# Optimization experiments

Hardware: AMD Instinct MI355X
Metric: run time of the kernel (lower is better)

## Reference

```python
import jax, jax.numpy as jnp
import numpy as np

B, V, F = 32, 1024, 16
A, P, NF = 32, 64, 128
C = P + A  # propagated feature width after concat with edge weights
D_OUT_IN = F + A + 2 * A * C  # 6192, input dim of output Dense


def setup_inputs() -> dict:
    key = jax.random.key(0)
    ks = jax.random.split(key, 4)
    return {
        "x": jax.random.normal(ks[0], (B, V, F), dtype=jnp.float32),
        "W_flr": jax.random.normal(ks[1], (F, P), dtype=jnp.float32) * (1.0 / np.sqrt(F)),
        "b_flr": jnp.zeros((P,), dtype=jnp.float32),
        "W_s": jax.random.normal(ks[2], (F, A), dtype=jnp.float32) * (1.0 / np.sqrt(F)),
        "b_s": jnp.zeros((A,), dtype=jnp.float32),
        "W_out": jax.random.normal(ks[3], (D_OUT_IN, NF), dtype=jnp.float32) * (1.0 / np.sqrt(D_OUT_IN)),
        "b_out": jnp.zeros((NF,), dtype=jnp.float32),
    }


def reference(x, W_flr, b_flr, W_s, b_s, W_out, b_out):
    # Per-vertex transforms
    feat = x @ W_flr + b_flr                      # (B,V,P)
    dist = x @ W_s + b_s                          # (B,V,A)
    ew = jnp.exp(-jnp.square(dist))               # (B,V,A) edge weights vertex->aggregator
    f = jnp.concatenate([feat, ew], axis=-1)      # (B,V,C)

    # Weighted broadcast then vertex-axis reduction (aggregator gather)
    w = jnp.transpose(ew, (0, 2, 1))              # (B,A,V)
    prod = w[..., None] * f[:, None, :, :]        # (B,A,V,C)
    agg_max = jnp.max(prod, axis=2)               # (B,A,C)
    agg_mean = jnp.mean(prod, axis=2)             # (B,A,C)
    agg = jnp.concatenate([agg_max, agg_mean], axis=-1)  # (B,A,2C)

    # Scatter aggregated features back to vertices, weighted by same edge weights
    upd = ew[..., None] * agg[:, None, :, :]      # (B,V,A,2C)
    upd = upd.reshape(B, V, A * 2 * C)            # (B,V,2AC)

    cat = jnp.concatenate([x, upd, ew], axis=-1)  # (B,V,F+2AC+A)
    return jnp.tanh(cat @ W_out + b_out)          # (B,V,NF)
```

## Files before the change

### kernel.cpp

```cpp
#include <hip/hip_runtime.h>
#include <hip/hip_bf16.h>
#include <math.h>

#define NB 32
#define NV 1024
#define NFT 16
#define NA 32
#define NP 64
#define NOUT 128
#define NC 96
#define NC2 192

#define NSPLIT 16
#define VPB 64

typedef __attribute__((ext_vector_type(8))) short bf16x8;
typedef __attribute__((ext_vector_type(4))) float f32x4;

__global__ void k2p(const float* __restrict__ x,
                    const float* __restrict__ W_flr,
                    const float* __restrict__ b_flr,
                    const float* __restrict__ W_s,
                    const float* __restrict__ b_s,
                    float* __restrict__ ewbuf,
                    float* __restrict__ part) {
    __shared__ float xs[VPB][NFT];
    __shared__ float fs[VPB][NC];

    int b = blockIdx.x, vs = blockIdx.y, tid = threadIdx.x;
    int rowbase = b * NV + vs * VPB;

    {
        const float4* xsrc = (const float4*)(x + (size_t)rowbase * NFT);
        ((float4*)xs)[tid] = xsrc[tid];
    }
    __syncthreads();

    {
        int c  = tid & 127;
        int rh = tid >> 7;
        if (c < NC) {
            float Wcol[NFT], bias;
            if (c < NP) {
                bias = b_flr[c];
#pragma unroll
                for (int k = 0; k < NFT; ++k) Wcol[k] = W_flr[k * NP + c];
            } else {
                int a = c - NP;
                bias = b_s[a];
#pragma unroll
                for (int k = 0; k < NFT; ++k) Wcol[k] = W_s[k * NA + a];
            }
#pragma unroll
            for (int r0 = 0; r0 < 32; ++r0) {
                int r = rh * 32 + r0;
                float xr[NFT];
#pragma unroll
                for (int q = 0; q < 4; ++q)
                    ((float4*)xr)[q] = ((const float4*)xs[r])[q];
                float acc = bias;
#pragma unroll
                for (int k = 0; k < NFT; ++k)
                    acc = fmaf(xr[k], Wcol[k], acc);
                if (c >= NP) {
                    acc = __expf(-acc * acc);
                    ewbuf[(size_t)(rowbase + r) * NA + (c - NP)] = acc;
                }
                fs[r][c] = acc;
            }
        }
    }
    __syncthreads();

    int at = tid >> 5, ct = tid & 31;
    int cbase = ct * 3;
    float sm[4][3], mx[4][3];
#pragma unroll
    for (int i = 0; i < 4; ++i)
#pragma unroll
        for (int j = 0; j < 3; ++j) { sm[i][j] = 0.f; mx[i][j] = -INFINITY; }

    for (int r = 0; r < VPB; ++r) {
        float4 e4 = *(const float4*)&fs[r][NP + at * 4];
        float f0 = fs[r][cbase], f1 = fs[r][cbase + 1], f2 = fs[r][cbase + 2];
        float ee[4] = {e4.x, e4.y, e4.z, e4.w};
#pragma unroll
        for (int i = 0; i < 4; ++i) {
            float p0 = ee[i] * f0, p1 = ee[i] * f1, p2 = ee[i] * f2;
            sm[i][0] += p0; sm[i][1] += p1; sm[i][2] += p2;
            mx[i][0] = fmaxf(mx[i][0], p0);
            mx[i][1] = fmaxf(mx[i][1], p1);
            mx[i][2] = fmaxf(mx[i][2], p2);
        }
    }

    float* pb = part + (size_t)((b * NSPLIT + vs) * NA) * NC2;
#pragma unroll
    for (int i = 0; i < 4; ++i) {
        int a = at * 4 + i;
#pragma unroll
        for (int j = 0; j < 3; ++j) {
            pb[a * NC2 + cbase + j]      = mx[i][j];
            pb[a * NC2 + NC + cbase + j] = sm[i][j];
        }
    }
}

__global__ void k23(const float* __restrict__ part,
                    const float* __restrict__ W_out,
                    float* __restrict__ Gp) {
    __shared__ float aggL[NC2];
    int b = blockIdx.x, a = blockIdx.y, tid = threadIdx.x;

    {
        const float* pb = part + (size_t)(b * NSPLIT * NA + a) * NC2 + tid;
        const size_t stride = (size_t)NA * NC2;
        if (tid < NC) {
            float m = -INFINITY;
#pragma unroll
            for (int vsi = 0; vsi < NSPLIT; ++vsi)
                m = fmaxf(m, pb[vsi * stride]);
            aggL[tid] = m;
        } else {
            float s = 0.f;
#pragma unroll
            for (int vsi = 0; vsi < NSPLIT; ++vsi)
                s += pb[vsi * stride];
            aggL[tid] = s * (1.0f / (float)NV);
        }
    }
    __syncthreads();

    if (tid < NOUT) {
        int n = tid;
        const float* wr = W_out + (size_t)(NFT + a * NC2) * NOUT + n;
        float acc = W_out[(size_t)(NFT + NA * NC2 + a) * NOUT + n];
#pragma unroll 8
        for (int c = 0; c < NC2; ++c)
            acc = fmaf(aggL[c], wr[(size_t)c * NOUT], acc);
        Gp[(size_t)(b * NA + a) * NOUT + n] = acc;
    }
}

#define MB 64
#define SWZ(r, k) (((r) << 6) + ((k) ^ (((r) & 7) << 3)))

__device__ inline void f2hl(float v, ushort& h, ushort& l) {
    __hip_bfloat16 hb = __float2bfloat16(v);
    float hf = __bfloat162float(hb);
    __hip_bfloat16 lb = __float2bfloat16(v - hf);
    h = *(ushort*)&hb;
    l = *(ushort*)&lb;
}

__global__ void k4_mfma(const float* __restrict__ x,
                        const float* __restrict__ ewbuf,
                        const float* __restrict__ Gp,
                        const float* __restrict__ W_out,
                        const float* __restrict__ b_out,
                        float* __restrict__ out) {
    __shared__ ushort AsH[MB * 64], AsL[MB * 64];
    __shared__ ushort BsH[NOUT * 64], BsL[NOUT * 64];
    __shared__ float  bs[NOUT];

    int rb = blockIdx.x;
    int b  = blockIdx.y;
    int tid = threadIdx.x;
    int rowbase = b * NV + rb * MB;

    {
        float4 v = ((const float4*)(x + (size_t)rowbase * NFT))[tid];
        int r = tid >> 2, kq = (tid & 3) * 4;
        float vv[4] = {v.x, v.y, v.z, v.w};
        ushort h[4], l[4];
#pragma unroll
        for (int j = 0; j < 4; ++j) f2hl(vv[j], h[j], l[j]);
        *(uint*)&AsH[SWZ(r, kq)]     = (uint)h[0] | ((uint)h[1] << 16);
        *(uint*)&AsH[SWZ(r, kq + 2)] = (uint)h[2] | ((uint)h[3] << 16);
        *(uint*)&AsL[SWZ(r, kq)]     = (uint)l[0] | ((uint)l[1] << 16);
        *(uint*)&AsL[SWZ(r, kq + 2)] = (uint)l[2] | ((uint)l[3] << 16);
    }
    {
        const float4* es4 = (const float4*)(ewbuf + (size_t)rowbase * NA);
#pragma unroll
        for (int t = 0; t < 2; ++t) {
            int i = tid * 2 + t;
            float4 v = es4[i];
            int r = i >> 3, kq = 16 + (i & 7) * 4;
            float vv[4] = {v.x, v.y, v.z, v.w};
            ushort h[4], l[4];
#pragma unroll
            for (int j = 0; j < 4; ++j) f2hl(vv[j], h[j], l[j]);
            *(uint*)&AsH[SWZ(r, kq)]     = (uint)h[0] | ((uint)h[1] << 16);
            *(uint*)&AsH[SWZ(r, kq + 2)] = (uint)h[2] | ((uint)h[3] << 16);
            *(uint*)&AsL[SWZ(r, kq)]     = (uint)l[0] | ((uint)l[1] << 16);
            *(uint*)&AsL[SWZ(r, kq + 2)] = (uint)l[2] | ((uint)l[3] << 16);
        }
    }
    {
#pragma unroll
        for (int t = 0; t < 2; ++t) {
            int i = tid * 2 + t;
            int r = i >> 3, kq = 48 + (i & 7) * 2;
            *(uint*)&AsH[SWZ(r, kq)] = 0u;
            *(uint*)&AsL[SWZ(r, kq)] = 0u;
        }
    }
    {
#pragma unroll
        for (int t = 0; t < 2; ++t) {
            int i = tid * 2 + t;
            int k = i >> 5, nq = (i & 31) * 4;
            float4 v = ((const float4*)W_out)[i];
            float vv[4] = {v.x, v.y, v.z, v.w};
#pragma unroll
            for (int j = 0; j < 4; ++j) {
                ushort h, l;
                f2hl(vv[j], h, l);
                BsH[SWZ(nq + j, k)] = h;
                BsL[SWZ(nq + j, k)] = l;
            }
        }
    }
    {
        const float4* gp4 = (const float4*)(Gp + (size_t)b * NA * NOUT);
#pragma unroll
        for (int t = 0; t < 4; ++t) {
            int i = tid * 4 + t;
            int a = i >> 5, nq = (i & 31) * 4;
            float4 v = gp4[i];
            int k = 16 + a;
            float vv[4] = {v.x, v.y, v.z, v.w};
#pragma unroll
            for (int j = 0; j < 4; ++j) {
                ushort h, l;
                f2hl(vv[j], h, l);
                BsH[SWZ(nq + j, k)] = h;
                BsL[SWZ(nq + j, k)] = l;
            }
        }
    }
    {
#pragma unroll
        for (int t = 0; t < 4; ++t) {
            int i = tid * 4 + t;
            int n = i >> 3, kq = 48 + (i & 7) * 2;
            *(uint*)&BsH[SWZ(n, kq)] = 0u;
            *(uint*)&BsL[SWZ(n, kq)] = 0u;
        }
    }
    if (tid < NOUT) bs[tid] = b_out[tid];

    __syncthreads();

    int w = tid >> 6, lane = tid & 63;
    int r16 = lane & 15, kg = lane >> 4, k0 = kg * 8;
    int arow = w * 16 + r16;

    bf16x8 AH0 = *(const bf16x8*)&AsH[SWZ(arow, k0)];
    bf16x8 AH1 = *(const bf16x8*)&AsH[SWZ(arow, 32 + k0)];
    bf16x8 AL0 = *(const bf16x8*)&AsL[SWZ(arow, k0)];
    bf16x8 AL1 = *(const bf16x8*)&AsL[SWZ(arow, 32 + k0)];

    int orow0 = rowbase + w * 16 + kg * 4;

#pragma unroll
    for (int nt = 0; nt < 8; ++nt) {
        int n = nt * 16 + r16;
        bf16x8 BH0 = *(const bf16x8*)&BsH[SWZ(n, k0)];
        bf16x8 BH1 = *(const bf16x8*)&BsH[SWZ(n, 32 + k0)];
        bf16x8 BL0 = *(const bf16x8*)&BsL[SWZ(n, k0)];
        bf16x8 BL1 = *(const bf16x8*)&BsL[SWZ(n, 32 + k0)];
        float bias = bs[n];
        f32x4 acc = {bias, bias, bias, bias};
        acc = __builtin_amdgcn_mfma_f32_16x16x32_bf16(AH0, BH0, acc, 0, 0, 0);
        acc = __builtin_amdgcn_mfma_f32_16x16x32_bf16(AL0, BH0, acc, 0, 0, 0);
        acc = __builtin_amdgcn_mfma_f32_16x16x32_bf16(AH0, BL0, acc, 0, 0, 0);
        acc = __builtin_amdgcn_mfma_f32_16x16x32_bf16(AH1, BH1, acc, 0, 0, 0);
        acc = __builtin_amdgcn_mfma_f32_16x16x32_bf16(AL1, BH1, acc, 0, 0, 0);
        acc = __builtin_amdgcn_mfma_f32_16x16x32_bf16(AH1, BL1, acc, 0, 0, 0);
#pragma unroll
        for (int rg = 0; rg < 4; ++rg) {
            float s = acc[rg];
            s = fminf(fmaxf(s, -15.f), 15.f);
            float e = __expf(2.f * s);
            out[(size_t)(orow0 + rg) * NOUT + n] =
                (e - 1.f) * __builtin_amdgcn_rcpf(e + 1.f);
        }
    }
}

extern "C" void kernel_launch(void* const* d_in, const int* in_sizes, int n_in,
                              void* d_out, int out_size, void* d_ws, size_t ws_size,
                              hipStream_t stream) {
    const float* x     = (const float*)d_in[0];
    const float* W_flr = (const float*)d_in[1];
    const float* b_flr = (const float*)d_in[2];
    const float* W_s   = (const float*)d_in[3];
    const float* b_s   = (const float*)d_in[4];
    const float* W_out = (const float*)d_in[5];
    const float* b_out = (const float*)d_in[6];
    float* out = (float*)d_out;

    float* ewbuf = (float*)d_ws;
    float* part  = ewbuf + (size_t)NB * NV * NA;
    float* Gp    = part  + (size_t)NB * NSPLIT * NA * NC2;

    {
        dim3 g(NB, NSPLIT);
        k2p<<<g, 256, 0, stream>>>(x, W_flr, b_flr, W_s, b_s, ewbuf, part);
    }
    {
        dim3 g(NB, NA);
        k23<<<g, 192, 0, stream>>>(part, W_out, Gp);
    }
    {
        dim3 g(NV / MB, NB);
        k4_mfma<<<g, 256, 0, stream>>>(x, ewbuf, Gp, W_out, b_out, out);
    }
}
```

Baseline: 41.19 us.

## Split vertex aggregation across thread halves with 4x6 register tiles and LDS combine

Result: faster. 38.58 us (-6.3%).

```diff
diff --git a/kernel.cpp b/kernel.cpp
--- a/kernel.cpp
+++ b/kernel.cpp
@@ -26,6 +26,7 @@
                     float* __restrict__ part) {
     __shared__ float xs[VPB][NFT];
     __shared__ float fs[VPB][NC];
+    __shared__ float pcomb[(31 * 100 + 95) * 2 + 2];
 
     int b = blockIdx.x, vs = blockIdx.y, tid = threadIdx.x;
     int rowbase = b * NV + vs * VPB;
@@ -72,36 +73,71 @@
     }
     __syncthreads();
 
-    int at = tid >> 5, ct = tid & 31;
-    int cbase = ct * 3;
-    float sm[4][3], mx[4][3];
+    int grp = tid >> 7;
+    int gl  = tid & 127;
+    int at = gl >> 4, ct = gl & 15;
+    int a0 = at * 4, c0 = ct * 6;
+    int rbase = grp * 32;
+
+    float sm[4][6], mx[4][6];
 #pragma unroll
     for (int i = 0; i < 4; ++i)
 #pragma unroll
-        for (int j = 0; j < 3; ++j) { sm[i][j] = 0.f; mx[i][j] = -INFINITY; }
-
-    for (int r = 0; r < VPB; ++r) {
-        float4 e4 = *(const float4*)&fs[r][NP + at * 4];
-        float f0 = fs[r][cbase], f1 = fs[r][cbase + 1], f2 = fs[r][cbase + 2];
+        for (int j = 0; j < 6; ++j) { sm[i][j] = 0.f; mx[i][j] = -INFINITY; }
+
+#pragma unroll 4
+    for (int r0 = 0; r0 < 32; ++r0) {
+        int r = rbase + r0;
+        float4 e4 = *(const float4*)&fs[r][NP + a0];
+        float2 fA = *(const float2*)&fs[r][c0];
+        float2 fB = *(const float2*)&fs[r][c0 + 2];
+        float2 fC = *(const float2*)&fs[r][c0 + 4];
+        float ff[6] = {fA.x, fA.y, fB.x, fB.y, fC.x, fC.y};
         float ee[4] = {e4.x, e4.y, e4.z, e4.w};
 #pragma unroll
+        for (int i = 0; i < 4; ++i)
+#pragma unroll
+            for (int j = 0; j < 6; ++j) {
+                float p = ee[i] * ff[j];
+                sm[i][j] += p;
+                mx[i][j] = fmaxf(mx[i][j], p);
+            }
+    }
+
+    if (grp == 0) {
+#pragma unroll
         for (int i = 0; i < 4; ++i) {
-            float p0 = ee[i] * f0, p1 = ee[i] * f1, p2 = ee[i] * f2;
-            sm[i][0] += p0; sm[i][1] += p1; sm[i][2] += p2;
-            mx[i][0] = fmaxf(mx[i][0], p0);
-            mx[i][1] = fmaxf(mx[i][1], p1);
-            mx[i][2] = fmaxf(mx[i][2], p2);
-        }
-    }
-
-    float* pb = part + (size_t)((b * NSPLIT + vs) * NA) * NC2;
-#pragma unroll
-    for (int i = 0; i < 4; ++i) {
-        int a = at * 4 + i;
-#pragma unroll
-        for (int j = 0; j < 3; ++j) {
-            pb[a * NC2 + cbase + j]      = mx[i][j];
-            pb[a * NC2 + NC + cbase + j] = sm[i][j];
+            int base = ((a0 + i) * 100 + c0) * 2;
+#pragma unroll
+            for (int q = 0; q < 3; ++q) {
+                float4 v = {sm[i][2 * q], mx[i][2 * q], sm[i][2 * q + 1], mx[i][2 * q + 1]};
+                *(float4*)&pcomb[base + q * 4] = v;
+            }
+        }
+    }
+    __syncthreads();
+    if (grp == 1) {
+        float* pb = part + (size_t)((b * NSPLIT + vs) * NA) * NC2;
+#pragma unroll
+        for (int i = 0; i < 4; ++i) {
+            int base = ((a0 + i) * 100 + c0) * 2;
+            float osm[6], omx[6];
+#pragma unroll
+            for (int q = 0; q < 3; ++q) {
+                float4 v = *(const float4*)&pcomb[base + q * 4];
+                osm[2 * q] = v.x; omx[2 * q] = v.y;
+                osm[2 * q + 1] = v.z; omx[2 * q + 1] = v.w;
+            }
+            int a = a0 + i;
+#pragma unroll
+            for (int q = 0; q < 3; ++q) {
+                float2 vm = {fmaxf(mx[i][2 * q], omx[2 * q]),
+                             fmaxf(mx[i][2 * q + 1], omx[2 * q + 1])};
+                float2 vsum = {sm[i][2 * q] + osm[2 * q],
+                               sm[i][2 * q + 1] + osm[2 * q + 1]};
+                *(float2*)&pb[a * NC2 + c0 + 2 * q]      = vm;
+                *(float2*)&pb[a * NC2 + NC + c0 + 2 * q] = vsum;
+            }
         }
     }
 }
@@ -143,7 +179,8 @@
 }
 
 #define MB 64
-#define SWZ(r, k) (((r) << 6) + ((k) ^ (((r) & 7) << 3)))
+#define SWZ(r, k)  (((r) << 6) + ((k) ^ (((r) & 7) << 3)))
+#define SWZB(n, k) (((n) << 6) + ((k) ^ (((((n) >> 3) & 7) ^ ((n) & 7)) << 3)))
 
 __device__ inline void f2hl(float v, ushort& h, ushort& l) {
     __hip_bfloat16 hb = __float2bfloat16(v);
@@ -217,8 +254,8 @@
             for (int j = 0; j < 4; ++j) {
                 ushort h, l;
                 f2hl(vv[j], h, l);
-                BsH[SWZ(nq + j, k)] = h;
-                BsL[SWZ(nq + j, k)] = l;
+                BsH[SWZB(nq + j, k)] = h;
+                BsL[SWZB(nq + j, k)] = l;
             }
         }
     }
@@ -235,8 +272,8 @@
             for (int j = 0; j < 4; ++j) {
                 ushort h, l;
                 f2hl(vv[j], h, l);
-                BsH[SWZ(nq + j, k)] = h;
-                BsL[SWZ(nq + j, k)] = l;
+                BsH[SWZB(nq + j, k)] = h;
+                BsL[SWZB(nq + j, k)] = l;
             }
         }
     }
@@ -245,8 +282,8 @@
         for (int t = 0; t < 4; ++t) {
             int i = tid * 4 + t;
             int n = i >> 3, kq = 48 + (i & 7) * 2;
-            *(uint*)&BsH[SWZ(n, kq)] = 0u;
-            *(uint*)&BsL[SWZ(n, kq)] = 0u;
+            *(uint*)&BsH[SWZB(n, kq)] = 0u;
+            *(uint*)&BsL[SWZB(n, kq)] = 0u;
         }
     }
     if (tid < NOUT) bs[tid] = b_out[tid];
@@ -267,10 +304,10 @@
 #pragma unroll
     for (int nt = 0; nt < 8; ++nt) {
         int n = nt * 16 + r16;
-        bf16x8 BH0 = *(const bf16x8*)&BsH[SWZ(n, k0)];
-        bf16x8 BH1 = *(const bf16x8*)&BsH[SWZ(n, 32 + k0)];
-        bf16x8 BL0 = *(const bf16x8*)&BsL[SWZ(n, k0)];
-        bf16x8 BL1 = *(const bf16x8*)&BsL[SWZ(n, 32 + k0)];
+        bf16x8 BH0 = *(const bf16x8*)&BsH[SWZB(n, k0)];
+        bf16x8 BH1 = *(const bf16x8*)&BsH[SWZB(n, 32 + k0)];
+        bf16x8 BL0 = *(const bf16x8*)&BsL[SWZB(n, k0)];
+        bf16x8 BL1 = *(const bf16x8*)&BsL[SWZB(n, 32 + k0)];
         float bias = bs[n];
         f32x4 acc = {bias, bias, bias, bias};
         acc = __builtin_amdgcn_mfma_f32_16x16x32_bf16(AH0, BH0, acc, 0, 0, 0);
```
